# Kernel tuning notes

Measured on AMD Instinct MI355X. Metric: run time of the kernel, lower is better.

## Reference

```python
import jax, jax.numpy as jnp
import numpy as np

H = 4096      # num_patches (sequence length)
WS = 8        # window_size
SHIFT = 4     # shift_size
NH = 8        # num_heads
DIM = 512     # embedding dim
HD = DIM // NH
NW = H // WS  # windows per batch element
B = 16
LN_EPS = 1e-5


def _layer_norm(x, g, b):
    m = jnp.mean(x, axis=-1, keepdims=True)
    v = jnp.var(x, axis=-1, keepdims=True)
    return (x - m) * jax.lax.rsqrt(v + LN_EPS) * g + b


def _window_partition(x):
    # Faithful to the repo: reshape->permute(nW<->ws)->flatten, giving strided windows.
    Bx, N, C = x.shape
    return x.reshape(Bx, N // WS, WS, C).transpose(0, 2, 1, 3).reshape(-1, WS, C)


def _window_reverse(w, N, Bx):
    C = w.shape[-1]
    return w.reshape(Bx, N // WS, WS, C).transpose(0, 2, 1, 3).reshape(Bx, N, C)


def _attn_mask():
    # Built exactly as in __init__ (numpy, constant at trace time): (NW, WS, WS)
    m = np.zeros((1, H, 1), np.float32)
    m[:, :H - WS] = 0.0
    m[:, H - WS:H - SHIFT] = 1.0
    m[:, H - SHIFT:] = 2.0
    mw = m.reshape(1, NW, WS, 1).transpose(0, 2, 1, 3).reshape(-1, WS)  # (NW, WS)
    d = mw[:, None, :] - mw[:, :, None]
    return np.where(d != 0, np.float32(-100.0), np.float32(0.0))


def _forward(x, norm1_g, norm1_b, qkv_w, qkv_b, proj_w, proj_b,
             norm2_g, norm2_b, fc1_w, fc1_b, fc2_w, fc2_b):
    Bx = x.shape[0]
    shortcut = x
    xn = _layer_norm(x, norm1_g, norm1_b)
    xs = jnp.roll(xn, -SHIFT, axis=1)
    xw = _window_partition(xs)                       # (Bx*NW, WS, DIM)
    B_ = xw.shape[0]
    qkv = xw @ qkv_w.T + qkv_b                       # (B_, WS, 3*DIM)
    qkv = qkv.reshape(B_, WS, 3, NH, HD).transpose(2, 0, 3, 1, 4)
    q, k, v = qkv[0], qkv[1], qkv[2]                 # (B_, NH, WS, HD)
    attn = jnp.einsum('bhqd,bhkd->bhqk', q, k) * (HD ** -0.5)
    mask = jnp.asarray(_attn_mask())                 # (NW, WS, WS)
    attn = attn.reshape(B_ // NW, NW, NH, WS, WS) + mask[None, :, None]
    attn = jax.nn.softmax(attn.reshape(B_, NH, WS, WS), axis=-1)
    o = jnp.einsum('bhqk,bhkd->bqhd', attn, v).reshape(B_, WS, DIM)
    o = o @ proj_w.T + proj_b
    xr = _window_reverse(o, H, Bx)
    xr = jnp.roll(xr, SHIFT, axis=1)
    x1 = shortcut + xr
    h = _layer_norm(x1, norm2_g, norm2_b)
    h = jax.nn.gelu(h @ fc1_w.T + fc1_b, approximate=False)
    h = h @ fc2_w.T + fc2_b
    return x1 + h


def setup_inputs() -> dict:
    key = jax.random.key(0)
    ks = jax.random.split(key, 8)
    s = 0.02
    return {
        'x': jax.random.normal(ks[0], (B, H, DIM), jnp.float32),
        'norm1_g': jnp.ones((DIM,), jnp.float32),
        'norm1_b': jnp.zeros((DIM,), jnp.float32),
        'qkv_w': jax.random.normal(ks[1], (3 * DIM, DIM), jnp.float32) * s,
        'qkv_b': jnp.zeros((3 * DIM,), jnp.float32),
        'proj_w': jax.random.normal(ks[2], (DIM, DIM), jnp.float32) * s,
        'proj_b': jnp.zeros((DIM,), jnp.float32),
        'norm2_g': jnp.ones((DIM,), jnp.float32),
        'norm2_b': jnp.zeros((DIM,), jnp.float32),
        'fc1_w': jax.random.normal(ks[3], (4 * DIM, DIM), jnp.float32) * s,
        'fc1_b': jnp.zeros((4 * DIM,), jnp.float32),
        'fc2_w': jax.random.normal(ks[4], (DIM, 4 * DIM), jnp.float32) * s,
        'fc2_b': jnp.zeros((DIM,), jnp.float32),
    }


def reference(x, norm1_g, norm1_b, qkv_w, qkv_b, proj_w, proj_b,
              norm2_g, norm2_b, fc1_w, fc1_b, fc2_w, fc2_b):
    return _forward(x, norm1_g, norm1_b, qkv_w, qkv_b, proj_w, proj_b,
                    norm2_g, norm2_b, fc1_w, fc1_b, fc2_w, fc2_b)
```

## Files before the change

kernel.cpp:

```cpp
#include <hip/hip_runtime.h>
#include <hip/hip_bf16.h>
#include <math.h>

typedef unsigned short ushortT;
typedef __attribute__((ext_vector_type(8))) short short8;
typedef __attribute__((ext_vector_type(4))) short short4v;
typedef __attribute__((ext_vector_type(4))) float f32x4;
typedef __attribute__((ext_vector_type(4))) float float4v;

#define TOK 65536
#define NSEQ 4096
#define DIM 512

__device__ __forceinline__ float bf2f(ushortT u) {
  union { float f; unsigned int i; } v; v.i = ((unsigned int)u) << 16; return v.f;
}
__device__ __forceinline__ ushortT f2bf(float f) {
  union { float f; unsigned int i; } v; v.f = f;
  unsigned int r = v.i + 0x7fffu + ((v.i >> 16) & 1u);
  return (ushortT)(r >> 16);
}

__device__ __forceinline__ float fast_gelu(float x) {
  const float y = fabsf(x) * 0.70710678118654752f;
  const float t = __builtin_amdgcn_rcpf(__builtin_fmaf(0.3275911f, y, 1.f));
  float p = 1.061405429f;
  p = __builtin_fmaf(p, t, -1.453152027f);
  p = __builtin_fmaf(p, t, 1.421413741f);
  p = __builtin_fmaf(p, t, -0.284496736f);
  p = __builtin_fmaf(p, t, 0.254829592f);
  p = p * t;
  const float e = __builtin_amdgcn_exp2f(-y * y * 1.4426950408889634f);
  float erfv = __builtin_fmaf(-p, e, 1.f);
  erfv = copysignf(erfv, x);
  return 0.5f * x * (1.f + erfv);
}

#define GLOAD_LDS(gp, lp) __builtin_amdgcn_global_load_lds( \
    (const __attribute__((address_space(1))) unsigned int*)(gp), \
    (__attribute__((address_space(3))) unsigned int*)(lp), 16, 0, 0)

#define BAR __builtin_amdgcn_s_barrier()
#define VMC(n) asm volatile("s_waitcnt vmcnt(" #n ")" ::: "memory")
#define SB0 __builtin_amdgcn_sched_barrier(0)

__global__ void cvt_kernel(const float* __restrict__ in, ushortT* __restrict__ out, int n4) {
  int i = blockIdx.x * 256 + threadIdx.x;
  if (i >= n4) return;
  float4v v = *(const float4v*)(in + (size_t)i * 4);
  short4v o;
#pragma unroll
  for (int j = 0; j < 4; ++j) o[j] = (short)f2bf(v[j]);
  *(short4v*)(out + (size_t)i * 4) = o;
}

template <bool INBF>
__global__ __launch_bounds__(256)
void ln_kernel(const void* __restrict__ inp, const float* __restrict__ gw,
               const float* __restrict__ bw, ushortT* __restrict__ out)
{
  const int lane = threadIdx.x & 63;
  const size_t tok = (size_t)blockIdx.x * 4 + (threadIdx.x >> 6);
  const int col = lane * 8;
  float x[8];
  if constexpr (INBF) {
    short8 v = *(const short8*)((const ushortT*)inp + tok * DIM + col);
#pragma unroll
    for (int j = 0; j < 8; ++j) x[j] = bf2f((ushortT)v[j]);
  } else {
    const float* p = (const float*)inp + tok * DIM + col;
    float4v a = *(const float4v*)p, b = *(const float4v*)(p + 4);
#pragma unroll
    for (int j = 0; j < 4; ++j) { x[j] = a[j]; x[4 + j] = b[j]; }
  }
  float s = 0.f, ss = 0.f;
#pragma unroll
  for (int j = 0; j < 8; ++j) { s += x[j]; ss += x[j] * x[j]; }
#pragma unroll
  for (int off = 1; off < 64; off <<= 1) {
    s += __shfl_xor(s, off, 64);
    ss += __shfl_xor(ss, off, 64);
  }
  const float mean = s * (1.f / 512.f);
  const float var = ss * (1.f / 512.f) - mean * mean;
  const float rstd = rsqrtf(var + 1e-5f);
  float4v g1 = *(const float4v*)(gw + col), g2 = *(const float4v*)(gw + col + 4);
  float4v b1 = *(const float4v*)(bw + col), b2 = *(const float4v*)(bw + col + 4);
  short8 o;
#pragma unroll
  for (int j = 0; j < 4; ++j) {
    o[j]     = (short)f2bf((x[j]     - mean) * rstd * g1[j] + b1[j]);
    o[4 + j] = (short)f2bf((x[4 + j] - mean) * rstd * g2[j] + b2[j]);
  }
  *(short8*)(out + tok * DIM + col) = o;
}

#define MFMA_PHASE(MH) \
  _Pragma("unroll") \
  for (int m_ = 0; m_ < 4; ++m_) \
    _Pragma("unroll") \
    for (int n_ = 0; n_ < 4; ++n_) \
      acc[(MH) * 4 + m_][n_] = __builtin_amdgcn_mfma_f32_16x16x32_bf16( \
          Af[m_], Bf[n_], acc[(MH) * 4 + m_][n_], 0, 0, 0)

#define STAGE_A2(bufp, h, gptr) do { \
    GLOAD_LDS((gptr) + (size_t)((h) * 128) * K,     (bufp) + (h) * 8192 + w * 1024); \
    GLOAD_LDS((gptr) + (size_t)((h) * 128 + 8) * K, (bufp) + (h) * 8192 + w * 1024 + 512); \
  } while (0)
#define STAGE_B2(bufp, h, gptr) do { \
    GLOAD_LDS((gptr) + (size_t)((h) * 128) * K,     (bufp) + (h) * 8192 + w * 1024); \
    GLOAD_LDS((gptr) + (size_t)((h) * 128 + 8) * K, (bufp) + (h) * 8192 + w * 1024 + 512); \
  } while (0)

template <int EPI>
__global__ __launch_bounds__(512, 2)
void gemm256(const ushortT* __restrict__ A, const ushortT* __restrict__ Bt,
             const float* __restrict__ bias, int M, int N, int K,
             ushortT* __restrict__ outb, float* __restrict__ outf,
             const float* __restrict__ resf, const ushortT* __restrict__ resb)
{
  __shared__ __align__(16) ushortT sm[65536];
  ushortT* const Ab0 = sm;
  ushortT* const Ab1 = sm + 16384;
  ushortT* const Bb0 = sm + 32768;
  ushortT* const Bb1 = sm + 49152;

  const int tid = threadIdx.x;
  const int w = tid >> 6, l = tid & 63;
  const int wr = w >> 2, wc = w & 3;

  const int nwg = gridDim.x * gridDim.y;
  int wg = blockIdx.y * gridDim.x + blockIdx.x;
  {
    const int q = nwg >> 3, r8 = nwg & 7;
    const int xc = wg & 7, yc = wg >> 3;
    wg = (xc < r8 ? xc * (q + 1) : r8 * (q + 1) + (xc - r8) * q) + yc;
  }
  const int nbn = N >> 8;
  const int mb = wg / nbn, nb = wg % nbn;
  const int m0 = mb << 8, n0 = nb << 8;
  const int NT = K >> 6;

  const ushortT* gA = A  + (size_t)(m0 + w * 16 + (l >> 3)) * K + (((l & 7) ^ (l >> 3)) << 3);
  const ushortT* gB = Bt + (size_t)(n0 + w * 16 + (l >> 3)) * K + (((l & 7) ^ (l >> 3)) << 3);

  const int rl = l & 15, ql = l >> 4;
  const int aoff = (wr * 128 + rl) * 64;
  const int boff = (wc * 64 + rl) * 64;
  const int cs0 = ((ql) ^ (l & 7)) << 3;
  const int cs1 = ((4 + ql) ^ (l & 7)) << 3;

  f32x4 acc[8][4];
  const f32x4 zero = {0.f, 0.f, 0.f, 0.f};
#pragma unroll
  for (int i = 0; i < 8; ++i)
#pragma unroll
    for (int j = 0; j < 4; ++j) acc[i][j] = zero;

  ushortT* Ac = Ab0; ushortT* An = Ab1;
  ushortT* Bc = Bb0; ushortT* Bn = Bb1;

  STAGE_A2(Ac, 0, gA); STAGE_A2(Ac, 1, gA);
  STAGE_B2(Bc, 0, gB); STAGE_B2(Bc, 1, gB);
  VMC(0);
  BAR;
  SB0;

  short8 Af[4], Bf[4];
  size_t koff = 64;

  for (int t = 0; t < NT; ++t) {
    if (t + 1 < NT) {
      STAGE_A2(An, 0, gA + koff); STAGE_A2(An, 1, gA + koff);
      STAGE_B2(Bn, 0, gB + koff); STAGE_B2(Bn, 1, gB + koff);
    }
#pragma unroll
    for (int m = 0; m < 4; ++m) Af[m] = *(const short8*)(Ac + aoff + m * 1024 + cs0);
#pragma unroll
    for (int n = 0; n < 4; ++n) Bf[n] = *(const short8*)(Bc + boff + n * 1024 + cs0);
    MFMA_PHASE(0);
#pragma unroll
    for (int m = 0; m < 4; ++m) Af[m] = *(const short8*)(Ac + aoff + (4 + m) * 1024 + cs0);
    MFMA_PHASE(1);
#pragma unroll
    for (int m = 0; m < 4; ++m) Af[m] = *(const short8*)(Ac + aoff + m * 1024 + cs1);
#pragma unroll
    for (int n = 0; n < 4; ++n) Bf[n] = *(const short8*)(Bc + boff + n * 1024 + cs1);
    MFMA_PHASE(0);
#pragma unroll
    for (int m = 0; m < 4; ++m) Af[m] = *(const short8*)(Ac + aoff + (4 + m) * 1024 + cs1);
    MFMA_PHASE(1);
    if (t + 1 < NT) VMC(0);
    BAR;
    SB0;
    ushortT* tp;
    tp = Ac; Ac = An; An = tp;
    tp = Bc; Bc = Bn; Bn = tp;
    koff += 64;
  }

  float* const ep = (float*)sm;
#pragma unroll
  for (int p = 0; p < 2; ++p) {
    if (p) BAR;
    if (wr == p) {
#pragma unroll
      for (int m = 0; m < 8; ++m) {
#pragma unroll
        for (int n = 0; n < 4; ++n) {
          const int c = wc * 64 + n * 16 + rl;
          const int pc = c ^ (c >> 3);
          *(f32x4*)(ep + (m * 4 + ql) * 1024 + pc * 4) = acc[m][n];
        }
      }
    }
    BAR;
#pragma unroll
    for (int k = 0; k < 4; ++k) {
      const int rb = w + k * 8;
      const int rowb = 16 * (rb >> 2) + 4 * (rb & 3);
      f32x4 rv[4];
#pragma unroll
      for (int j = 0; j < 4; ++j) {
        const int c = 4 * l + j;
        const int pc = c ^ (c >> 3);
        rv[j] = *(const f32x4*)(ep + rb * 1024 + pc * 4);
      }
      const int col = n0 + 4 * l;
      const float4v bb = *(const float4v*)(bias + col);
#pragma unroll
      for (int i = 0; i < 4; ++i) {
        const size_t row = (size_t)(m0 + p * 128 + rowb + i);
        float v0 = rv[0][i] + bb[0], v1 = rv[1][i] + bb[1],
              v2 = rv[2][i] + bb[2], v3 = rv[3][i] + bb[3];
        if constexpr (EPI == 1) {
          const float4v rr = *(const float4v*)(resf + row * (size_t)N + col);
          v0 += rr[0]; v1 += rr[1]; v2 += rr[2]; v3 += rr[3];
        }
        if constexpr (EPI == 2) {
          v0 = fast_gelu(v0); v1 = fast_gelu(v1); v2 = fast_gelu(v2); v3 = fast_gelu(v3);
        }
        if constexpr (EPI == 3) {
          const short4v rb4 = *(const short4v*)(resb + row * (size_t)N + col);
          v0 += bf2f((ushortT)rb4[0]); v1 += bf2f((ushortT)rb4[1]);
          v2 += bf2f((ushortT)rb4[2]); v3 += bf2f((ushortT)rb4[3]);
          float4v o = {v0, v1, v2, v3};
          *(float4v*)(outf + row * (size_t)N + col) = o;
        } else {
          short4v o;
          o[0] = (short)f2bf(v0); o[1] = (short)f2bf(v1);
          o[2] = (short)f2bf(v2); o[3] = (short)f2bf(v3);
          *(short4v*)(outb + row * (size_t)N + col) = o;
        }
      }
    }
  }
}

__global__ __launch_bounds__(512)
void attn_kernel(const ushortT* __restrict__ qkv, ushortT* __restrict__ out)
{
  __shared__ __align__(16) ushortT sq[8][1544];
  const int wb = blockIdx.x;
  const int b  = wb >> 9;
  const int rr = wb & 511;
  const int w1 = rr >> 6;
  const int g  = rr & 63;
  const int tid = threadIdx.x;

#pragma unroll
  for (int c = 0; c < 3; ++c) {
    const int f = c * 512 + tid;
    const int i = f / 192;
    const int col = (f % 192) * 8;
    const int tin = (64 * g + 8 * i + w1 + 4) & (NSEQ - 1);
    const ushortT* src = qkv + ((size_t)b * NSEQ + tin) * 1536 + col;
    *(short8*)(&sq[i][col]) = *(const short8*)src;
  }
  __syncthreads();

  const int wave = tid >> 6, lane = tid & 63;
  const int h = wave;
  const int qi = lane >> 3, kj = lane & 7;

  float s = 0.f;
  const ushortT* qrow = &sq[qi][h * 64];
  const ushortT* krow = &sq[kj][512 + h * 64];
#pragma unroll
  for (int c = 0; c < 8; ++c) {
    short8 qa = *(const short8*)(qrow + c * 8);
    short8 ka = *(const short8*)(krow + c * 8);
#pragma unroll
    for (int j = 0; j < 8; ++j) s += bf2f((ushortT)qa[j]) * bf2f((ushortT)ka[j]);
  }
  s *= 0.125f;

  const int pq = 64 * g + 8 * qi + w1;
  const int pk = 64 * g + 8 * kj + w1;
  const int cq = (pq < 4088) ? 0 : (pq < 4092 ? 1 : 2);
  const int ck = (pk < 4088) ? 0 : (pk < 4092 ? 1 : 2);
  if (cq != ck) s -= 100.f;

  float mx = s;
  mx = fmaxf(mx, __shfl_xor(mx, 1, 64));
  mx = fmaxf(mx, __shfl_xor(mx, 2, 64));
  mx = fmaxf(mx, __shfl_xor(mx, 4, 64));
  const float e = expf(s - mx);
  float sum = e;
  sum += __shfl_xor(sum, 1, 64);
  sum += __shfl_xor(sum, 2, 64);
  sum += __shfl_xor(sum, 4, 64);
  const float p = e / sum;

  const int dc = lane & 7;
  float o[8];
#pragma unroll
  for (int j = 0; j < 8; ++j) o[j] = 0.f;
#pragma unroll
  for (int k2 = 0; k2 < 8; ++k2) {
    const float pk2 = __shfl(p, (lane & ~7) + k2, 64);
    short8 va = *(const short8*)(&sq[k2][1024 + h * 64 + dc * 8]);
#pragma unroll
    for (int j = 0; j < 8; ++j) o[j] += pk2 * bf2f((ushortT)va[j]);
  }

  const int tout = (512 * qi + 64 * w1 + g + 4) & (NSEQ - 1);
  short8 ov;
#pragma unroll
  for (int j = 0; j < 8; ++j) ov[j] = (short)f2bf(o[j]);
  *(short8*)(out + ((size_t)b * NSEQ + tout) * DIM + h * 64 + dc * 8) = ov;
}

extern "C" void kernel_launch(void* const* d_in, const int* in_sizes, int n_in,
                              void* d_out, int out_size, void* d_ws, size_t ws_size,
                              hipStream_t stream) {
  const float* x      = (const float*)d_in[0];
  const float* n1g    = (const float*)d_in[1];
  const float* n1b    = (const float*)d_in[2];
  const float* qkv_w  = (const float*)d_in[3];
  const float* qkv_b  = (const float*)d_in[4];
  const float* proj_w = (const float*)d_in[5];
  const float* proj_b = (const float*)d_in[6];
  const float* n2g    = (const float*)d_in[7];
  const float* n2b    = (const float*)d_in[8];
  const float* fc1_w  = (const float*)d_in[9];
  const float* fc1_b  = (const float*)d_in[10];
  const float* fc2_w  = (const float*)d_in[11];
  const float* fc2_b  = (const float*)d_in[12];
  float* out = (float*)d_out;

  size_t off = 0;
  char* ws = (char*)d_ws;
  auto alloc = [&](size_t b) { void* p = ws + off; off += (b + 255) & ~(size_t)255; return p; };

  ushortT* qkvw_b = (ushortT*)alloc((size_t)1536 * 512 * 2);
  ushortT* projw_b = (ushortT*)alloc((size_t)512 * 512 * 2);
  ushortT* fc1w_b = (ushortT*)alloc((size_t)2048 * 512 * 2);
  ushortT* fc2w_b = (ushortT*)alloc((size_t)512 * 2048 * 2);
  ushortT* bufA = (ushortT*)alloc((size_t)TOK * 512 * 2);
  ushortT* bufQ = (ushortT*)alloc((size_t)TOK * 1536 * 2);
  ushortT* x1 = bufQ;

  int nch = 1;
  while (nch < 16) {
    size_t need = (size_t)(TOK / nch) * 2048 * 2;
    if (off + need <= ws_size) break;
    nch <<= 1;
  }
  ushortT* h1 = (ushortT*)(ws + off);

  cvt_kernel<<<(1536 * 512 / 4 + 255) / 256, 256, 0, stream>>>(qkv_w, qkvw_b, 1536 * 512 / 4);
  cvt_kernel<<<(512 * 512 / 4 + 255) / 256, 256, 0, stream>>>(proj_w, projw_b, 512 * 512 / 4);
  cvt_kernel<<<(2048 * 512 / 4 + 255) / 256, 256, 0, stream>>>(fc1_w, fc1w_b, 2048 * 512 / 4);
  cvt_kernel<<<(512 * 2048 / 4 + 255) / 256, 256, 0, stream>>>(fc2_w, fc2w_b, 512 * 2048 / 4);

  ln_kernel<false><<<TOK / 4, 256, 0, stream>>>(x, n1g, n1b, bufA);

  gemm256<0><<<dim3(TOK / 256, 1536 / 256), 512, 0, stream>>>(
      bufA, qkvw_b, qkv_b, TOK, 1536, 512, bufQ, nullptr, nullptr, nullptr);

  attn_kernel<<<8192, 512, 0, stream>>>(bufQ, bufA);

  gemm256<1><<<dim3(TOK / 256, 512 / 256), 512, 0, stream>>>(
      bufA, projw_b, proj_b, TOK, 512, 512, x1, nullptr, x, nullptr);

  ln_kernel<true><<<TOK / 4, 256, 0, stream>>>(x1, n2g, n2b, bufA);

  const int tc = TOK / nch;
  for (int c = 0; c < nch; ++c) {
    const ushortT* hin = bufA + (size_t)c * tc * 512;
    gemm256<2><<<dim3(tc / 256, 2048 / 256), 512, 0, stream>>>(
        hin, fc1w_b, fc1_b, tc, 2048, 512, h1, nullptr, nullptr, nullptr);
    gemm256<3><<<dim3(tc / 256, 512 / 256), 512, 0, stream>>>(
        h1, fc2w_b, fc2_b, tc, 512, 2048, nullptr, out + (size_t)c * tc * 512,
        nullptr, x1 + (size_t)c * tc * 512);
  }
}
```

Measured before the change: 681.0 us.

## Deepen GEMM mainloop to 4-stage K=32 pipeline with new LDS swizzle

The GEMM main loop moves from a double-buffered K=64 tile to a four-slot ring of K=32 tiles, keeping three loads in flight ahead of compute. Each wave now stages 32 rows with a new XOR swizzle, and the finer-grained vmcnt waits only block on the oldest stage. The goal is to hide global-to-LDS latency behind MFMA work, at the cost of twice as many iterations and barriers per K, plus more A-fragment registers (8 instead of 4).

```diff
diff --git a/kernel.cpp b/kernel.cpp
--- a/kernel.cpp
+++ b/kernel.cpp
@@ -95,21 +95,13 @@
   *(short8*)(out + tok * DIM + col) = o;
 }
 
-#define MFMA_PHASE(MH) \
-  _Pragma("unroll") \
-  for (int m_ = 0; m_ < 4; ++m_) \
-    _Pragma("unroll") \
-    for (int n_ = 0; n_ < 4; ++n_) \
-      acc[(MH) * 4 + m_][n_] = __builtin_amdgcn_mfma_f32_16x16x32_bf16( \
-          Af[m_], Bf[n_], acc[(MH) * 4 + m_][n_], 0, 0, 0)
-
-#define STAGE_A2(bufp, h, gptr) do { \
-    GLOAD_LDS((gptr) + (size_t)((h) * 128) * K,     (bufp) + (h) * 8192 + w * 1024); \
-    GLOAD_LDS((gptr) + (size_t)((h) * 128 + 8) * K, (bufp) + (h) * 8192 + w * 1024 + 512); \
-  } while (0)
-#define STAGE_B2(bufp, h, gptr) do { \
-    GLOAD_LDS((gptr) + (size_t)((h) * 128) * K,     (bufp) + (h) * 8192 + w * 1024); \
-    GLOAD_LDS((gptr) + (size_t)((h) * 128 + 8) * K, (bufp) + (h) * 8192 + w * 1024 + 512); \
+#define STG(bA, bB, kt) do { \
+    const ushortT* _ga = gA + (size_t)(kt) * 32; \
+    const ushortT* _gb = gB + (size_t)(kt) * 32; \
+    GLOAD_LDS(_ga,                  (bA) + w * 1024); \
+    GLOAD_LDS(_ga + (size_t)16 * K, (bA) + w * 1024 + 512); \
+    GLOAD_LDS(_gb,                  (bB) + w * 1024); \
+    GLOAD_LDS(_gb + (size_t)16 * K, (bB) + w * 1024 + 512); \
   } while (0)
 
 template <int EPI>
@@ -120,10 +112,6 @@
              const float* __restrict__ resf, const ushortT* __restrict__ resb)
 {
   __shared__ __align__(16) ushortT sm[65536];
-  ushortT* const Ab0 = sm;
-  ushortT* const Ab1 = sm + 16384;
-  ushortT* const Bb0 = sm + 32768;
-  ushortT* const Bb1 = sm + 49152;
 
   const int tid = threadIdx.x;
   const int w = tid >> 6, l = tid & 63;
@@ -139,16 +127,16 @@
   const int nbn = N >> 8;
   const int mb = wg / nbn, nb = wg % nbn;
   const int m0 = mb << 8, n0 = nb << 8;
-  const int NT = K >> 6;
-
-  const ushortT* gA = A  + (size_t)(m0 + w * 16 + (l >> 3)) * K + (((l & 7) ^ (l >> 3)) << 3);
-  const ushortT* gB = Bt + (size_t)(n0 + w * 16 + (l >> 3)) * K + (((l & 7) ^ (l >> 3)) << 3);
+  const int NT = K >> 5;
+
+  const int scw = ((l & 3) ^ ((l >> 2) & 3) ^ (l >> 4)) << 3;
+  const ushortT* gA = A  + (size_t)(m0 + w * 32 + (l >> 2)) * K + scw;
+  const ushortT* gB = Bt + (size_t)(n0 + w * 32 + (l >> 2)) * K + scw;
 
   const int rl = l & 15, ql = l >> 4;
-  const int aoff = (wr * 128 + rl) * 64;
-  const int boff = (wc * 64 + rl) * 64;
-  const int cs0 = ((ql) ^ (l & 7)) << 3;
-  const int cs1 = ((4 + ql) ^ (l & 7)) << 3;
+  const int xr = (rl & 3) ^ ((rl >> 2) & 3);
+  const int aoff = (wr * 128 + rl) * 32 + ((ql ^ xr) << 3);
+  const int boff = (wc * 64 + rl) * 32 + ((ql ^ xr) << 3);
 
   f32x4 acc[8][4];
   const f32x4 zero = {0.f, 0.f, 0.f, 0.f};
@@ -157,46 +145,38 @@
 #pragma unroll
     for (int j = 0; j < 4; ++j) acc[i][j] = zero;
 
-  ushortT* Ac = Ab0; ushortT* An = Ab1;
-  ushortT* Bc = Bb0; ushortT* Bn = Bb1;
-
-  STAGE_A2(Ac, 0, gA); STAGE_A2(Ac, 1, gA);
-  STAGE_B2(Bc, 0, gB); STAGE_B2(Bc, 1, gB);
-  VMC(0);
-  BAR;
-  SB0;
-
-  short8 Af[4], Bf[4];
-  size_t koff = 64;
+  ushortT* a0 = sm;              ushortT* b0 = sm + 8192;
+  ushortT* a1 = sm + 16384;      ushortT* b1 = sm + 24576;
+  ushortT* a2 = sm + 32768;      ushortT* b2 = sm + 40960;
+  ushortT* a3 = sm + 49152;      ushortT* b3 = sm + 57344;
+
+  STG(a0, b0, 0);
+  STG(a1, b1, 1);
+  STG(a2, b2, 2);
+  VMC(8);
+  BAR; SB0;
+
+  short8 Af[8], Bf[4];
 
   for (int t = 0; t < NT; ++t) {
-    if (t + 1 < NT) {
-      STAGE_A2(An, 0, gA + koff); STAGE_A2(An, 1, gA + koff);
-      STAGE_B2(Bn, 0, gB + koff); STAGE_B2(Bn, 1, gB + koff);
-    }
-#pragma unroll
-    for (int m = 0; m < 4; ++m) Af[m] = *(const short8*)(Ac + aoff + m * 1024 + cs0);
-#pragma unroll
-    for (int n = 0; n < 4; ++n) Bf[n] = *(const short8*)(Bc + boff + n * 1024 + cs0);
-    MFMA_PHASE(0);
-#pragma unroll
-    for (int m = 0; m < 4; ++m) Af[m] = *(const short8*)(Ac + aoff + (4 + m) * 1024 + cs0);
-    MFMA_PHASE(1);
-#pragma unroll
-    for (int m = 0; m < 4; ++m) Af[m] = *(const short8*)(Ac + aoff + m * 1024 + cs1);
-#pragma unroll
-    for (int n = 0; n < 4; ++n) Bf[n] = *(const short8*)(Bc + boff + n * 1024 + cs1);
-    MFMA_PHASE(0);
-#pragma unroll
-    for (int m = 0; m < 4; ++m) Af[m] = *(const short8*)(Ac + aoff + (4 + m) * 1024 + cs1);
-    MFMA_PHASE(1);
-    if (t + 1 < NT) VMC(0);
-    BAR;
+    if (t + 3 < NT) STG(a3, b3, t + 3);
+#pragma unroll
+    for (int m = 0; m < 8; ++m) Af[m] = *(const short8*)(a0 + aoff + m * 512);
+#pragma unroll
+    for (int n = 0; n < 4; ++n) Bf[n] = *(const short8*)(b0 + boff + n * 512);
+#pragma unroll
+    for (int m = 0; m < 8; ++m)
+#pragma unroll
+      for (int n = 0; n < 4; ++n)
+        acc[m][n] = __builtin_amdgcn_mfma_f32_16x16x32_bf16(Af[m], Bf[n], acc[m][n], 0, 0, 0);
     SB0;
+    if (t + 4 <= NT)      { VMC(8); }
+    else if (t + 3 == NT) { VMC(4); }
+    else if (t + 2 == NT) { VMC(0); }
+    BAR; SB0;
     ushortT* tp;
-    tp = Ac; Ac = An; An = tp;
-    tp = Bc; Bc = Bn; Bn = tp;
-    koff += 64;
+    tp = a0; a0 = a1; a1 = a2; a2 = a3; a3 = tp;
+    tp = b0; b0 = b1; b1 = b2; b2 = b3; b3 = tp;
   }
 
   float* const ep = (float*)sm;
```

After: 716.0 us. 1.05x slower.
